# Kernel optimization log

Measured on AMD Instinct MI355X. Metric: run time of the kernel, lower is better.

The kernel has to match this reference:

```python
import jax, jax.numpy as jnp
import numpy as np

EPS = 1e-5
SLOPE = 0.2  # leaky_relu negative_slope


def _mesh_conv_face(fe, gemm, w, b):
    # fe: [B, C, F]; gemm: [B, F, 3] neighbor face indices; w: [O, C, 4]; b: [O]
    # Gather 3 neighbor faces per face (irregular access).
    nb = jax.vmap(lambda f, g: f[:, g])(fe, gemm)  # [B, C, F, 3]
    n1, n2, n3 = nb[..., 0], nb[..., 1], nb[..., 2]
    # Symmetric (order-invariant) feature columns over the 3 neighbors.
    G = jnp.stack(
        [
            fe,                                                        # center face
            n1 + n2 + n3,                                              # sum
            jnp.abs(n1 - n2) + jnp.abs(n2 - n3) + jnp.abs(n3 - n1),    # pairwise abs-diff sum
            jnp.maximum(n1, jnp.maximum(n2, n3)),                      # max
        ],
        axis=-1,
    )  # [B, C, F, 4]
    # Conv2d with kernel (1,4) == contraction over (C, 4).
    return jnp.einsum('bcfk,ock->bof', G, w) + b[None, :, None]  # [B, O, F]


def _bn(x, gamma, beta):
    # BatchNorm2d (training mode) on [B, C, F]; normalize per-channel over (B, F).
    mu = x.mean(axis=(0, 2), keepdims=True)
    var = x.var(axis=(0, 2), keepdims=True)  # biased, as torch uses for normalization
    xn = (x - mu) * jax.lax.rsqrt(var + EPS)
    return gamma[None, :, None] * xn + beta[None, :, None]


def _lrelu(x):
    return jnp.where(x >= 0, x, SLOPE * x)


def setup_inputs() -> dict:
    key = jax.random.key(0)
    ks = jax.random.split(key, 8)
    B, Cin, Cout, F = 4, 32, 64, 50000
    fe = jax.random.normal(ks[0], (B, Cin, F), dtype=jnp.float32)
    gemm = jax.random.randint(ks[1], (B, F, 3), 0, F)
    w1 = jax.random.normal(ks[2], (Cout, Cin, 4), dtype=jnp.float32) * 0.05
    w2a = jax.random.normal(ks[3], (Cout, Cout, 4), dtype=jnp.float32) * 0.05
    w2b = jax.random.normal(ks[4], (Cout, Cout, 4), dtype=jnp.float32) * 0.05
    z = jnp.zeros((Cout,), jnp.float32)
    o = jnp.ones((Cout,), jnp.float32)
    return {
        'fe': fe, 'gemm': gemm,
        'w1': w1, 'b1': z, 'w2a': w2a, 'b2a': z, 'w2b': w2b, 'b2b': z,
        'g0': o, 'be0': z, 'g1': o, 'be1': z, 'g2': o, 'be2': z,
    }


def reference(fe, gemm, w1, b1, w2a, b2a, w2b, b2b, g0, be0, g1, be1, g2, be2):
    # conv1 -> BN -> LeakyReLU
    x1 = _lrelu(_bn(_mesh_conv_face(fe, gemm, w1, b1), g0, be0))
    # residual block 1
    x2 = _lrelu(_bn(_mesh_conv_face(x1, gemm, w2a, b2a), g1, be1) + x1)
    x1 = x2
    # residual block 2
    x2 = _lrelu(_bn(_mesh_conv_face(x1, gemm, w2b, b2b), g2, be2) + x1)
    return x2  # [B, Cout, F]; pool=0 so before_pool is None
```

## Files before the change

kernel.cpp:

```cpp
#include <hip/hip_runtime.h>
#include <hip/hip_bf16.h>
#include <math.h>


typedef __attribute__((ext_vector_type(8))) short short8;
typedef __attribute__((ext_vector_type(8))) unsigned short ushort8_t;
typedef __attribute__((ext_vector_type(4))) float f32x4;

__device__ inline unsigned short f2bf(float v) {
    union { float f; unsigned u; } x; x.f = v;
    unsigned r = x.u + 0x7fffu + ((x.u >> 16) & 1u);
    return (unsigned short)(r >> 16);
}
__device__ inline float bf2f(unsigned short u) {
    union { unsigned u; float f; } x; x.u = ((unsigned)u) << 16; return x.f;
}
__device__ inline unsigned pk2(float a, float b) {
    union { __hip_bfloat162 h; unsigned u; } c;
    c.h = __float22bfloat162_rn(make_float2(a, b));
    return c.u;
}

__global__ void transpose_fe_kernel(const float* __restrict__ fe,
                                    unsigned short* __restrict__ o, int F,
                                    const float* __restrict__ w1,
                                    const float* __restrict__ w2a,
                                    const float* __restrict__ w2b,
                                    unsigned short* __restrict__ w1b,
                                    unsigned short* __restrict__ w2ab,
                                    unsigned short* __restrict__ w2bb)
{
    __shared__ float tile[64 * 33];
    const int b = blockIdx.y;
    const int f0 = blockIdx.x * 64;
    const int t = threadIdx.x;

    {
        const int bid = blockIdx.y * gridDim.x + blockIdx.x;
        if (bid < 32)       { const int i = bid * 256 + t;        w1b[i]  = f2bf(w1[i]);  }
        else if (bid < 96)  { const int i = (bid - 32) * 256 + t; w2ab[i] = f2bf(w2a[i]); }
        else if (bid < 160) { const int i = (bid - 96) * 256 + t; w2bb[i] = f2bf(w2b[i]); }
    }

    const int lane = t & 63;
    const int w = t >> 6;
    const int f = f0 + lane;
    if (f < F) {
#pragma unroll
        for (int i = 0; i < 8; ++i) {
            const int c = w * 8 + i;
            tile[lane * 33 + c] = fe[((size_t)b * 32 + c) * F + f];
        }
    }
    __syncthreads();
    const int j = t >> 2, s = t & 3;
    const int fj = f0 + j;
    if (fj < F) {
        unsigned fw[4];
#pragma unroll
        for (int i = 0; i < 4; ++i)
            fw[i] = pk2(tile[j * 33 + s * 8 + 2 * i], tile[j * 33 + s * 8 + 2 * i + 1]);
        *(uint4*)(o + ((size_t)b * F + fj) * 32 + s * 8) = make_uint4(fw[0], fw[1], fw[2], fw[3]);
    }
}

template <int CIN, bool NORM>
__launch_bounds__(256, (CIN == 32) ? 5 : (NORM ? 3 : 4))
__global__ void conv_mfma_kernel(const unsigned short* __restrict__ x,
                                 const int*   __restrict__ gidx,
                                 const unsigned short* __restrict__ wb,
                                 const float* __restrict__ bias,
                                 const float* __restrict__ mrIn,
                                 unsigned short* __restrict__ y,
                                 float* __restrict__ pS,
                                 float* __restrict__ pQ,
                                 int nb, int nbx, int F)
{
    constexpr int NSEG = CIN / 32;
    constexpr int K    = 4 * CIN;
    constexpr int RB   = 2 * K;
    constexpr int GB   = 64 * RB;
    constexpr int GREG = (GB > 17408) ? GB : 17408;
    __shared__ __align__(16) unsigned char smem[GREG];
    float* tile = (float*)smem;

    const int NBg = gridDim.x;
    const int t = threadIdx.x;
    const int j = t >> 2, s = t & 3;
    const int lane = t & 63, wv = t >> 6;
    const int l15 = lane & 15, quad = lane >> 4;
    const int kb = quad * 8;

    unsigned char* grow = smem + j * RB;
    const int swz = (j & 7) << 4;

    short8 afr[K / 32];
    {
        const int ar = wv * 16 + l15;
#pragma unroll
        for (int ksi = 0; ksi < K / 32; ++ksi)
            afr[ksi] = *(const short8*)(wb + (size_t)ar * K + ksi * 32 + kb);
    }
    const f32x4 bias4 = *(const f32x4*)(bias + wv * 16 + quad * 4);

    float scr[NSEG * 8], shr[NSEG * 8];
    if constexpr (NORM) {
#pragma unroll
        for (int i = 0; i < NSEG; ++i) {
            const int c0 = (i * 4 + s) * 8;
#pragma unroll
            for (int h = 0; h < 2; ++h) {
                const f32x4 a  = *(const f32x4*)(mrIn + c0 + 4 * h);
                const f32x4 sh = *(const f32x4*)(mrIn + 64 + c0 + 4 * h);
#pragma unroll
                for (int q = 0; q < 4; ++q) {
                    scr[i * 8 + 4 * h + q] = a[q];
                    shr[i * 8 + 4 * h + q] = sh[q];
                }
            }
        }
    }

    ushort8_t vc[NSEG], v0[NSEG], v1[NSEG], v2[NSEG];
    int gA0, gA1, gA2;
    float S_acc = 0.f, Q_acc = 0.f;
    const int so = t & 63, sg = t >> 6;

    int tl = blockIdx.x;

    {
        const int b0 = tl / nbx;
        const int f0 = (tl - b0 * nbx) * 64;
        const int fc = min(f0 + j, F - 1);
        const int* gp = gidx + ((size_t)b0 * F + fc) * 3;
        const int g0 = gp[0], g1 = gp[1], g2 = gp[2];
        const unsigned short* xb = x + (size_t)b0 * F * CIN;
        const unsigned short* pc = xb + (size_t)fc * CIN;
        const unsigned short* p0 = xb + (size_t)g0 * CIN;
        const unsigned short* p1 = xb + (size_t)g1 * CIN;
        const unsigned short* p2 = xb + (size_t)g2 * CIN;
#pragma unroll
        for (int i = 0; i < NSEG; ++i) {
            const int c0 = (i * 4 + s) * 8;
            vc[i] = *(const ushort8_t*)(pc + c0);
            v0[i] = *(const ushort8_t*)(p0 + c0);
            v1[i] = *(const ushort8_t*)(p1 + c0);
            v2[i] = *(const ushort8_t*)(p2 + c0);
        }
    }
    {
        const int tn = min(tl + NBg, nb - 1);
        const int bn = tn / nbx;
        const int fn = min((tn - bn * nbx) * 64 + j, F - 1);
        const int* gp = gidx + ((size_t)bn * F + fn) * 3;
        gA0 = gp[0]; gA1 = gp[1]; gA2 = gp[2];
    }

    for (; tl < nb; tl += NBg) {
        const int b  = tl / nbx;
        const int f0 = (tl - b * nbx) * 64;

#pragma unroll
        for (int i = 0; i < NSEG; ++i) {
            const int c0 = (i * 4 + s) * 8;
            unsigned fw[16];
#pragma unroll
            for (int q = 0; q < 8; ++q) {
                float ctr = bf2f(vc[i][q]);
                float a   = bf2f(v0[i][q]);
                float bb  = bf2f(v1[i][q]);
                float cc  = bf2f(v2[i][q]);
                if constexpr (NORM) {
                    const float sc_ = scr[i * 8 + q], sh_ = shr[i * 8 + q];
                    ctr = fmaf(ctr, sc_, sh_); ctr = fmaxf(ctr, 0.2f * ctr);
                    a   = fmaf(a,   sc_, sh_); a   = fmaxf(a,   0.2f * a);
                    bb  = fmaf(bb,  sc_, sh_); bb  = fmaxf(bb,  0.2f * bb);
                    cc  = fmaf(cc,  sc_, sh_); cc  = fmaxf(cc,  0.2f * cc);
                }
                const float su = a + bb + cc;
                const float dd = fabsf(a - bb) + fabsf(bb - cc) + fabsf(cc - a);
                const float mm = fmaxf(a, fmaxf(bb, cc));
                fw[2 * q]     = pk2(ctr, su);
                fw[2 * q + 1] = pk2(dd, mm);
            }
#pragma unroll
            for (int q4 = 0; q4 < 4; ++q4) {
                const int qb = 8 * c0 + 16 * q4;
                *(uint4*)(grow + (qb ^ swz)) =
                    make_uint4(fw[4 * q4], fw[4 * q4 + 1], fw[4 * q4 + 2], fw[4 * q4 + 3]);
            }
        }

        {
            const int tn = min(tl + NBg, nb - 1);
            const int bn = tn / nbx;
            const int fcn = min((tn - bn * nbx) * 64 + j, F - 1);
            const unsigned short* xb = x + (size_t)bn * F * CIN;
            const unsigned short* pc = xb + (size_t)fcn * CIN;
            const unsigned short* p0 = xb + (size_t)gA0 * CIN;
            const unsigned short* p1 = xb + (size_t)gA1 * CIN;
            const unsigned short* p2 = xb + (size_t)gA2 * CIN;
#pragma unroll
            for (int i = 0; i < NSEG; ++i) {
                const int c0 = (i * 4 + s) * 8;
                vc[i] = *(const ushort8_t*)(pc + c0);
                v0[i] = *(const ushort8_t*)(p0 + c0);
                v1[i] = *(const ushort8_t*)(p1 + c0);
                v2[i] = *(const ushort8_t*)(p2 + c0);
            }
            const int t2 = min(tl + 2 * NBg, nb - 1);
            const int b2 = t2 / nbx;
            const int f2 = min((t2 - b2 * nbx) * 64 + j, F - 1);
            const int* gp = gidx + ((size_t)b2 * F + f2) * 3;
            gA0 = gp[0]; gA1 = gp[1]; gA2 = gp[2];
        }
        __syncthreads();

        f32x4 acc[4];
#pragma unroll
        for (int nt = 0; nt < 4; ++nt) acc[nt] = (f32x4){0.f, 0.f, 0.f, 0.f};
#pragma unroll
        for (int ksi = 0; ksi < K / 32; ++ksi) {
            const int cb = 2 * (ksi * 32 + kb);
#pragma unroll
            for (int nt = 0; nt < 4; ++nt) {
                const int nr = nt * 16 + l15;
                const short8 bfr = *(const short8*)(smem + nr * RB + (cb ^ ((nr & 7) << 4)));
                acc[nt] = __builtin_amdgcn_mfma_f32_16x16x32_bf16(afr[ksi], bfr, acc[nt], 0, 0, 0);
            }
        }
        __syncthreads();

        {
            const int cb0 = wv * 16 + quad * 4;
#pragma unroll
            for (int nt = 0; nt < 4; ++nt) {
                const int face = nt * 16 + l15;
                *(f32x4*)(tile + face * 68 + cb0) = acc[nt] + bias4;
            }
        }
        __syncthreads();
        {
#pragma unroll
            for (int i = 0; i < 16; ++i) {
                const int f = sg + 4 * i;
                if (f0 + f < F) {
                    const float v = tile[f * 68 + so];
                    S_acc += v; Q_acc += v * v;
                }
            }
        }
        {
            const int f = f0 + j;
            if (f < F) {
                unsigned fw[8];
#pragma unroll
                for (int ii = 0; ii < 8; ++ii)
                    fw[ii] = pk2(tile[j * 68 + s * 16 + 2 * ii],
                                 tile[j * 68 + s * 16 + 2 * ii + 1]);
                unsigned short* yp = y + ((size_t)b * F + f) * 64 + s * 16;
                *(uint4*)yp       = make_uint4(fw[0], fw[1], fw[2], fw[3]);
                *(uint4*)(yp + 8) = make_uint4(fw[4], fw[5], fw[6], fw[7]);
            }
        }
        __syncthreads();
    }

    float* redS = (float*)smem;
    float* redQ = redS + 256;
    redS[t] = S_acc; redQ[t] = Q_acc;
    __syncthreads();
    if (t < 64) {
        pS[(size_t)blockIdx.x * 64 + t] = redS[t] + redS[64 + t] + redS[128 + t] + redS[192 + t];
        pQ[(size_t)blockIdx.x * 64 + t] = redQ[t] + redQ[64 + t] + redQ[128 + t] + redQ[192 + t];
    }
}

__global__ void finalize_kernel(const float* __restrict__ pS, const float* __restrict__ pQ,
                                int nbg, float invN,
                                const float* __restrict__ gamma,
                                const float* __restrict__ beta,
                                float* __restrict__ mr)
{
    __shared__ float rs_[256], rq_[256];
    const int o = blockIdx.x, t = threadIdx.x;
    float S = 0.f, Q = 0.f;
    for (int jj = t; jj < nbg; jj += 256) {
        S += pS[(size_t)jj * 64 + o];
        Q += pQ[(size_t)jj * 64 + o];
    }
    rs_[t] = S; rq_[t] = Q;
    __syncthreads();
#pragma unroll
    for (int s = 128; s > 0; s >>= 1) {
        if (t < s) { rs_[t] += rs_[t + s]; rq_[t] += rq_[t + s]; }
        __syncthreads();
    }
    if (t == 0) {
        const float mu  = rs_[0] * invN;
        const float var = rq_[0] * invN - mu * mu;
        const float rsg = rsqrtf(var + 1e-5f);
        const float sc  = gamma[o] * rsg;
        mr[o]      = sc;
        mr[64 + o] = fmaf(-sc, mu, beta[o]);
    }
}

__global__ void norm_res_kernel(const unsigned short* __restrict__ y1,
                                const unsigned short* __restrict__ y2,
                                const float* __restrict__ mr1,
                                const float* __restrict__ mr2,
                                unsigned short* __restrict__ out,
                                int N8)
{
    const int tid = blockIdx.x * blockDim.x + threadIdx.x;
    if (tid >= N8) return;
    const int c0 = (tid & 7) * 8;
    const ushort8_t a = *(const ushort8_t*)(y1 + (size_t)tid * 8);
    const ushort8_t b = *(const ushort8_t*)(y2 + (size_t)tid * 8);
    float r[8];
#pragma unroll
    for (int h = 0; h < 2; ++h) {
        const f32x4 s1 = *(const f32x4*)(mr1 + c0 + 4 * h);
        const f32x4 h1 = *(const f32x4*)(mr1 + 64 + c0 + 4 * h);
        const f32x4 s2 = *(const f32x4*)(mr2 + c0 + 4 * h);
        const f32x4 h2 = *(const f32x4*)(mr2 + 64 + c0 + 4 * h);
#pragma unroll
        for (int i = 0; i < 4; ++i) {
            float x1 = fmaf(bf2f(a[4 * h + i]), s1[i], h1[i]);
            x1 = fmaxf(x1, 0.2f * x1);
            float v = fmaf(bf2f(b[4 * h + i]), s2[i], h2[i]) + x1;
            r[4 * h + i] = fmaxf(v, 0.2f * v);
        }
    }
    unsigned fw[4];
#pragma unroll
    for (int i = 0; i < 4; ++i) fw[i] = pk2(r[2 * i], r[2 * i + 1]);
    *(uint4*)(out + (size_t)tid * 8) = make_uint4(fw[0], fw[1], fw[2], fw[3]);
}

__global__ void norm_transpose_kernel(const unsigned short* __restrict__ y,
                                      const unsigned short* __restrict__ res,
                                      const float* __restrict__ mr,
                                      float* __restrict__ out, int F)
{
    __shared__ float tile[64 * 65];
    const int b = blockIdx.y, f0 = blockIdx.x * 64, t = threadIdx.x;
    const int j = t >> 2, s = t & 3;
    const int f = f0 + j;
    if (f < F) {
        const size_t row = ((size_t)b * F + f) * 64;
#pragma unroll
        for (int i = 0; i < 2; ++i) {
            const int c0 = s * 16 + i * 8;
            const ushort8_t yv = *(const ushort8_t*)(y + row + c0);
            const ushort8_t rv = *(const ushort8_t*)(res + row + c0);
#pragma unroll
            for (int h = 0; h < 2; ++h) {
                const f32x4 sc = *(const f32x4*)(mr + c0 + 4 * h);
                const f32x4 sh = *(const f32x4*)(mr + 64 + c0 + 4 * h);
#pragma unroll
                for (int q = 0; q < 4; ++q) {
                    float vv = fmaf(bf2f(yv[4 * h + q]), sc[q], sh[q]) + bf2f(rv[4 * h + q]);
                    vv = fmaxf(vv, 0.2f * vv);
                    tile[(c0 + 4 * h + q) * 65 + j] = vv;
                }
            }
        }
    }
    __syncthreads();
    const int o = t >> 2;
    float* ob = out + ((size_t)b * 64 + o) * F + f0;
#pragma unroll
    for (int i = 0; i < 4; ++i) {
        const int fs = (i * 4 + s) * 4;
        if (f0 + fs < F) {
            f32x4 v;
#pragma unroll
            for (int q = 0; q < 4; ++q) v[q] = tile[o * 65 + fs + q];
            *(f32x4*)(ob + fs) = v;
        }
    }
}

extern "C" void kernel_launch(void* const* d_in, const int* in_sizes, int n_in,
                              void* d_out, int out_size, void* d_ws, size_t ws_size,
                              hipStream_t stream)
{
    const float* fe  = (const float*)d_in[0];
    const int*   gm  = (const int*)d_in[1];
    const float* w1  = (const float*)d_in[2];
    const float* b1  = (const float*)d_in[3];
    const float* w2a = (const float*)d_in[4];
    const float* b2a = (const float*)d_in[5];
    const float* w2b = (const float*)d_in[6];
    const float* b2b = (const float*)d_in[7];
    const float* g0  = (const float*)d_in[8];
    const float* be0 = (const float*)d_in[9];
    const float* g1  = (const float*)d_in[10];
    const float* be1 = (const float*)d_in[11];
    const float* g2  = (const float*)d_in[12];
    const float* be2 = (const float*)d_in[13];

    const int B = 4, O = 64;
    const int F = in_sizes[0] / (B * 32);
    const int M = B * F;
    const float invN = 1.0f / (float)M;
    const int nbx = (F + 63) / 64;
    const int nb  = nbx * B;

    unsigned short* Y1 = (unsigned short*)d_ws;
    unsigned short* Y2 = Y1 + (size_t)M * O;
    unsigned short* x2 = Y2 + (size_t)M * O;
    float* pS  = (float*)(x2 + (size_t)M * O);
    float* pQ  = pS + 2048 * 64;
    float* mr1 = pQ + 2048 * 64;
    float* mr2 = mr1 + 128;
    float* mr3 = mr2 + 128;
    unsigned short* w1b  = (unsigned short*)(mr3 + 128);
    unsigned short* w2ab = w1b + 64 * 128;
    unsigned short* w2bb = w2ab + 64 * 256;
    unsigned short* fe_t = (unsigned short*)d_out;

    dim3 blk(256);
    dim3 tgrid(nbx, B);
    const int N8 = M * 8;
    dim3 ngrid((N8 + 255) / 256);
    const int g1g = (nb < 1280) ? nb : 1280;
    const int g2g = (nb < 768)  ? nb : 768;
    const int g3g = (nb < 1024) ? nb : 1024;

    transpose_fe_kernel<<<tgrid, blk, 0, stream>>>(fe, fe_t, F,
                                                   w1, w2a, w2b, w1b, w2ab, w2bb);

    conv_mfma_kernel<32, false><<<g1g, blk, 0, stream>>>(
        fe_t, gm, w1b, b1, nullptr, Y1, pS, pQ, nb, nbx, F);
    finalize_kernel<<<64, 256, 0, stream>>>(pS, pQ, g1g, invN, g0, be0, mr1);

    conv_mfma_kernel<64, true><<<g2g, blk, 0, stream>>>(
        Y1, gm, w2ab, b2a, mr1, Y2, pS, pQ, nb, nbx, F);
    finalize_kernel<<<64, 256, 0, stream>>>(pS, pQ, g2g, invN, g1, be1, mr2);

    norm_res_kernel<<<ngrid, blk, 0, stream>>>(Y1, Y2, mr1, mr2, x2, N8);

    conv_mfma_kernel<64, false><<<g3g, blk, 0, stream>>>(
        x2, gm, w2bb, b2b, nullptr, Y1, pS, pQ, nb, nbx, F);
    finalize_kernel<<<64, 256, 0, stream>>>(pS, pQ, g3g, invN, g2, be2, mr3);

    norm_transpose_kernel<<<tgrid, blk, 0, stream>>>(Y1, x2, mr3, (float*)d_out, F);
}
```

Measured before the change: 219.7 us.

## Write conv outputs directly from MFMA registers and reduce BN stats via shuffles

The epilogue no longer stages the accumulator tile through shared memory. Each lane writes its 4 bf16 outputs straight from the MFMA accumulators and keeps per-channel sum and sum-of-squares in registers, reducing them with xor shuffles across the 16 face lanes. Dropping the staging tile shrinks shared memory and removes several barriers, so launch bounds and persistent grid sizes are raised to run more blocks per CU. The trade-off is narrower 8-byte scattered global stores instead of 16-byte row stores, and possible register pressure at the higher occupancy target.

```diff
diff --git a/kernel.cpp b/kernel.cpp
--- a/kernel.cpp
+++ b/kernel.cpp
@@ -65,7 +65,7 @@
 }
 
 template <int CIN, bool NORM>
-__launch_bounds__(256, (CIN == 32) ? 5 : (NORM ? 3 : 4))
+__launch_bounds__(256, (CIN == 32) ? 8 : 5)
 __global__ void conv_mfma_kernel(const unsigned short* __restrict__ x,
                                  const int*   __restrict__ gidx,
                                  const unsigned short* __restrict__ wb,
@@ -80,9 +80,7 @@
     constexpr int K    = 4 * CIN;
     constexpr int RB   = 2 * K;
     constexpr int GB   = 64 * RB;
-    constexpr int GREG = (GB > 17408) ? GB : 17408;
-    __shared__ __align__(16) unsigned char smem[GREG];
-    float* tile = (float*)smem;
+    __shared__ __align__(16) unsigned char smem[GB];
 
     const int NBg = gridDim.x;
     const int t = threadIdx.x;
@@ -123,8 +121,7 @@
 
     ushort8_t vc[NSEG], v0[NSEG], v1[NSEG], v2[NSEG];
     int gA0, gA1, gA2;
-    float S_acc = 0.f, Q_acc = 0.f;
-    const int so = t & 63, sg = t >> 6;
+    f32x4 S4 = {0.f, 0.f, 0.f, 0.f}, Q4 = {0.f, 0.f, 0.f, 0.f};
 
     int tl = blockIdx.x;
 
@@ -231,48 +228,31 @@
         }
         __syncthreads();
 
-        {
-            const int cb0 = wv * 16 + quad * 4;
-#pragma unroll
-            for (int nt = 0; nt < 4; ++nt) {
-                const int face = nt * 16 + l15;
-                *(f32x4*)(tile + face * 68 + cb0) = acc[nt] + bias4;
-            }
-        }
-        __syncthreads();
-        {
-#pragma unroll
-            for (int i = 0; i < 16; ++i) {
-                const int f = sg + 4 * i;
-                if (f0 + f < F) {
-                    const float v = tile[f * 68 + so];
-                    S_acc += v; Q_acc += v * v;
-                }
-            }
-        }
-        {
-            const int f = f0 + j;
+#pragma unroll
+        for (int nt = 0; nt < 4; ++nt) {
+            const f32x4 av = acc[nt] + bias4;
+            const int f = f0 + nt * 16 + l15;
             if (f < F) {
-                unsigned fw[8];
-#pragma unroll
-                for (int ii = 0; ii < 8; ++ii)
-                    fw[ii] = pk2(tile[j * 68 + s * 16 + 2 * ii],
-                                 tile[j * 68 + s * 16 + 2 * ii + 1]);
-                unsigned short* yp = y + ((size_t)b * F + f) * 64 + s * 16;
-                *(uint4*)yp       = make_uint4(fw[0], fw[1], fw[2], fw[3]);
-                *(uint4*)(yp + 8) = make_uint4(fw[4], fw[5], fw[6], fw[7]);
-            }
-        }
-        __syncthreads();
-    }
-
-    float* redS = (float*)smem;
-    float* redQ = redS + 256;
-    redS[t] = S_acc; redQ[t] = Q_acc;
-    __syncthreads();
-    if (t < 64) {
-        pS[(size_t)blockIdx.x * 64 + t] = redS[t] + redS[64 + t] + redS[128 + t] + redS[192 + t];
-        pQ[(size_t)blockIdx.x * 64 + t] = redQ[t] + redQ[64 + t] + redQ[128 + t] + redQ[192 + t];
+                S4 += av;
+                Q4 += av * av;
+                unsigned short* yp = y + ((size_t)b * F + f) * 64 + wv * 16 + quad * 4;
+                *(uint2*)yp = make_uint2(pk2(av[0], av[1]), pk2(av[2], av[3]));
+            }
+        }
+    }
+
+#pragma unroll
+    for (int m = 1; m <= 8; m <<= 1) {
+#pragma unroll
+        for (int q = 0; q < 4; ++q) {
+            S4[q] += __shfl_xor(S4[q], m);
+            Q4[q] += __shfl_xor(Q4[q], m);
+        }
+    }
+    if (l15 == 0) {
+        const int c0 = wv * 16 + quad * 4;
+        *(f32x4*)(pS + (size_t)blockIdx.x * 64 + c0) = S4;
+        *(f32x4*)(pQ + (size_t)blockIdx.x * 64 + c0) = Q4;
     }
 }
 
@@ -426,9 +406,9 @@
     dim3 tgrid(nbx, B);
     const int N8 = M * 8;
     dim3 ngrid((N8 + 255) / 256);
-    const int g1g = (nb < 1280) ? nb : 1280;
-    const int g2g = (nb < 768)  ? nb : 768;
-    const int g3g = (nb < 1024) ? nb : 1024;
+    const int g1g = (nb < 2048) ? nb : 2048;
+    const int g2g = (nb < 1280) ? nb : 1280;
+    const int g3g = g2g;
 
     transpose_fe_kernel<<<tgrid, blk, 0, stream>>>(fe, fe_t, F,
                                                    w1, w2a, w2b, w1b, w2ab, w2bb);
```

After: 338.3 us. 54.0% more time.
